# Kernel tuning notes

Measured on AMD Instinct MI355X. Metric: run time of the kernel, lower is better.

## Reference

```python
import jax, jax.numpy as jnp
import numpy as np

D_MODEL = 1024
N_HEADS = 16
D_HEAD = D_MODEL // N_HEADS


def setup_inputs() -> dict:
    key = jax.random.key(0)
    ks = jax.random.split(key, 11)
    B, S = 2, 2048
    s_in = 1.0 / np.sqrt(D_MODEL)
    return {
        "query": jax.random.normal(ks[0], (B, S, D_MODEL), jnp.float32),
        "key": jax.random.normal(ks[1], (B, S, D_MODEL), jnp.float32),
        "value": jax.random.normal(ks[2], (B, S, D_MODEL), jnp.float32),
        "Wq_w": jax.random.normal(ks[3], (D_MODEL, D_MODEL), jnp.float32) * s_in,
        "Wq_b": jax.random.normal(ks[4], (D_MODEL,), jnp.float32) * 0.01,
        "Wk_w": jax.random.normal(ks[5], (D_HEAD, D_MODEL), jnp.float32) * s_in,
        "Wk_b": jax.random.normal(ks[6], (D_HEAD,), jnp.float32) * 0.01,
        "Wv_w": jax.random.normal(ks[7], (D_HEAD, D_MODEL), jnp.float32) * s_in,
        "Wv_b": jax.random.normal(ks[8], (D_HEAD,), jnp.float32) * 0.01,
        "Wo_w": jax.random.normal(ks[9], (D_MODEL, D_MODEL), jnp.float32) * s_in,
        "Wo_b": jax.random.normal(ks[10], (D_MODEL,), jnp.float32) * 0.01,
    }


def reference(query, key, value, Wq_w, Wq_b, Wk_w, Wk_b, Wv_w, Wv_b, Wo_w, Wo_b):
    B, S, _ = query.shape
    # Q: per-head projection [B, H, S, dh]; K/V: single shared head [B, S, dh]
    Q = (query @ Wq_w.T + Wq_b).reshape(B, S, N_HEADS, D_HEAD).transpose(0, 2, 1, 3)
    K = key @ Wk_w.T + Wk_b      # [B, S, dh], shared across heads (MQA)
    V = value @ Wv_w.T + Wv_b    # [B, S, dh]
    scale = 1.0 / np.sqrt(D_HEAD).astype(np.float32)
    scores = jnp.einsum('bhqd,bkd->bhqk', Q, K) * scale  # [B, H, S, S]
    attn = jax.nn.softmax(scores, axis=-1)
    ctx = jnp.einsum('bhqk,bkd->bhqd', attn, V)           # [B, H, S, dh]
    ctx = ctx.transpose(0, 2, 1, 3).reshape(B, S, D_MODEL)
    out = ctx @ Wo_w.T + Wo_b
    return out, attn
```

## Files before the change

### kernel.cpp

```cpp
#include <hip/hip_runtime.h>
#include <hip/hip_bf16.h>
#include <math.h>

#define D_MODEL 1024
#define N_HEADS 16
#define D_HEAD 64
#define S_ 2048

typedef __attribute__((ext_vector_type(8))) short short8;
typedef __attribute__((ext_vector_type(4))) float f32x4;
typedef __attribute__((ext_vector_type(16))) float f32x16;

static __device__ inline short f2bf(float f) {
    union { __hip_bfloat16 h; short s; } u;
    u.h = __float2bfloat16(f);
    return u.s;
}

static __device__ inline f32x4 mfma16(short8 a, short8 b, f32x4 c) {
    return __builtin_amdgcn_mfma_f32_16x16x32_bf16(a, b, c, 0, 0, 0);
}
static __device__ inline f32x16 mfma32(short8 a, short8 b, f32x16 c) {
    return __builtin_amdgcn_mfma_f32_32x32x16_bf16(a, b, c, 0, 0, 0);
}
static __device__ inline f32x16 zero16() {
    f32x16 z;
#pragma unroll
    for (int i = 0; i < 16; i++) z[i] = 0.f;
    return z;
}

static __device__ inline void load_lds16(const void* g, void* l) {
    __builtin_amdgcn_global_load_lds(
        (const __attribute__((address_space(1))) unsigned int*)g,
        (__attribute__((address_space(3))) unsigned int*)l, 16, 0, 0);
}

__global__ __launch_bounds__(256)
void cvt_all(const float* __restrict__ q, const float* __restrict__ k,
             const float* __restrict__ v, const float* __restrict__ wq,
             const float* __restrict__ wk, const float* __restrict__ wv,
             const float* __restrict__ wo,
             short* dq, short* dk, short* dv, short* dwq, short* dwk,
             short* dwv, short* dwo) {
    size_t c = (size_t)blockIdx.x * 256 + threadIdx.x;
    const float* s; short* d; size_t off;
    if (c < 524288)        { s = q;  d = dq;  off = c; }
    else if (c < 1048576)  { s = k;  d = dk;  off = c - 524288; }
    else if (c < 1572864)  { s = v;  d = dv;  off = c - 1048576; }
    else if (c < 1703936)  { s = wq; d = dwq; off = c - 1572864; }
    else if (c < 1712128)  { s = wk; d = dwk; off = c - 1703936; }
    else if (c < 1720320)  { s = wv; d = dwv; off = c - 1712128; }
    else                   { s = wo; d = dwo; off = c - 1720320; }
    const f32x4* sp = (const f32x4*)(s + off * 8);
    f32x4 a = sp[0], b = sp[1];
    short8 o;
    o[0] = f2bf(a[0]); o[1] = f2bf(a[1]); o[2] = f2bf(a[2]); o[3] = f2bf(a[3]);
    o[4] = f2bf(b[0]); o[5] = f2bf(b[1]); o[6] = f2bf(b[2]); o[7] = f2bf(b[3]);
    *(short8*)(d + off * 8) = o;
}

template<int BM, int BN, int OUT_MODE>
__device__ __forceinline__ void gemm_body(
    const short* __restrict__ A, const short* __restrict__ Wb,
    const float* __restrict__ bias, void* __restrict__ Cv,
    int bx, int by, int M, int N, int K, float out_scale, char* lds)
{
    constexpr int NI = BM / 32, NJ = BN / 32;
    constexpr int AISS = BM / 32, WISS = BN / 32;
    char* As = lds;
    char* Ws = lds + 2 * BM * 128;
    const int t = threadIdx.x, lane = t & 63, w = t >> 6;
    const int wr = w >> 1, wc = w & 1, r15 = lane & 15, g = lane >> 4;
    const int m0 = by * BM, n0 = bx * BN;
    const size_t Kb2 = (size_t)K * 2;

    int aR[AISS], aC[AISS];
#pragma unroll
    for (int i = 0; i < AISS; i++) {
        int l = i * 4096 + t * 16;
        aR[i] = l >> 7;
        aC[i] = (l & 127) ^ (((l >> 7) & 7) << 4);
    }

    f32x4 acc[NI][NJ];
#pragma unroll
    for (int i = 0; i < NI; i++)
#pragma unroll
        for (int j = 0; j < NJ; j++) acc[i][j] = (f32x4){0.f, 0.f, 0.f, 0.f};

    const int nk = K / 64;
    auto stage = [&](int kt, int buf) {
        size_t kb = (size_t)kt * 128;
#pragma unroll
        for (int i = 0; i < AISS; i++)
            load_lds16((const char*)A + (size_t)(m0 + aR[i]) * Kb2 + kb + aC[i],
                       As + buf * (BM * 128) + i * 4096 + (w << 10));
#pragma unroll
        for (int i = 0; i < WISS; i++)
            load_lds16((const char*)Wb + (size_t)(n0 + aR[i]) * Kb2 + kb + aC[i],
                       Ws + buf * (BN * 128) + i * 4096 + (w << 10));
    };

    stage(0, 0);
    __syncthreads();
    int cur = 0;
    for (int kt = 0; kt < nk; kt++) {
        if (kt + 1 < nk) stage(kt + 1, cur ^ 1);
        const char* Ab = As + cur * (BM * 128);
        const char* Wbs = Ws + cur * (BN * 128);
#pragma unroll
        for (int kc = 0; kc < 2; kc++) {
            short8 af[NI], bw[NJ];
#pragma unroll
            for (int i = 0; i < NI; i++) {
                int r = wr * (16 * NI) + i * 16 + r15;
                af[i] = *(const short8*)(Ab + r * 128 + ((kc * 64 + g * 16) ^ ((r & 7) << 4)));
            }
#pragma unroll
            for (int j = 0; j < NJ; j++) {
                int r = wc * (16 * NJ) + j * 16 + r15;
                bw[j] = *(const short8*)(Wbs + r * 128 + ((kc * 64 + g * 16) ^ ((r & 7) << 4)));
            }
#pragma unroll
            for (int i = 0; i < NI; i++)
#pragma unroll
                for (int j = 0; j < NJ; j++)
                    acc[i][j] = mfma16(af[i], bw[j], acc[i][j]);
        }
        __syncthreads();
        cur ^= 1;
    }

#pragma unroll
    for (int i = 0; i < NI; i++) {
#pragma unroll
        for (int j = 0; j < NJ; j++) {
            int ncol = n0 + wc * (16 * NJ) + j * 16 + r15;
            float bv = bias[ncol];
#pragma unroll
            for (int reg = 0; reg < 4; reg++) {
                int mrow = m0 + wr * (16 * NI) + i * 16 + g * 4 + reg;
                float val = (acc[i][j][reg] + bv) * out_scale;
                if (OUT_MODE == 0) {
                    __builtin_nontemporal_store(val, (float*)Cv + (size_t)mrow * N + ncol);
                } else if (OUT_MODE == 1) {
                    ((short*)Cv)[(size_t)mrow * N + ncol] = f2bf(val);
                } else {
                    ((short*)Cv)[((((size_t)(mrow >> 11)) * 64 + ncol) << 11) +
                                 (mrow & 2047)] = f2bf(val);
                }
            }
        }
    }
}

__global__ __launch_bounds__(256)
void qkv_proj(const short* __restrict__ qin, const short* __restrict__ kin,
              const short* __restrict__ vin, const short* __restrict__ wqb,
              const short* __restrict__ wkb, const short* __restrict__ wvb,
              const float* __restrict__ bq, const float* __restrict__ bk,
              const float* __restrict__ bv,
              short* Qb, short* Kb, short* Vtb) {
    __shared__ char lds[65536];
    int bid = blockIdx.x;
    if (bid < 256)
        gemm_body<128, 128, 1>(qin, wqb, bq, Qb, bid & 7, bid >> 3,
                               4096, 1024, 1024, 0.18033688011112f, lds);
    else if (bid < 288)
        gemm_body<128, 64, 1>(kin, wkb, bk, Kb, 0, bid - 256,
                              4096, 64, 1024, 1.0f, lds);
    else
        gemm_body<128, 64, 2>(vin, wvb, bv, Vtb, 0, bid - 288,
                              4096, 64, 1024, 1.0f, lds);
}

__global__ __launch_bounds__(256)
void o_proj(const short* __restrict__ ctxb, const short* __restrict__ wob,
            const float* __restrict__ bo, float* __restrict__ out) {
    __shared__ char lds[65536];
    gemm_body<128, 128, 0>(ctxb, wob, bo, out, blockIdx.x & 7, blockIdx.x >> 3,
                           4096, 1024, 1024, 1.0f, lds);
}

__global__ __launch_bounds__(256)
void mqa_attn3(const short* __restrict__ Qb,
               const short* __restrict__ Kb,
               const short* __restrict__ Vtb,
               float* __restrict__ attn,
               short* __restrict__ ctxb)
{
    __shared__ short KB2[2][64 * 64];
    __shared__ short VB2[2][64 * 64];
    __shared__ short Ps[128 * 64];

    const int t = threadIdx.x, lane = t & 63, w = t >> 6;
    const int l31 = lane & 31, h5 = lane >> 5;
    const int bid = blockIdx.x;
    const int qt = bid & 15, h = (bid >> 4) & 15, b = bid >> 8;
    const int q0 = qt * 128;
    const int wq = w * 32;

    short8 aq[4];
    {
        const char* qbase = (const char*)(Qb +
            (size_t)(b * S_ + q0 + wq + l31) * D_MODEL + h * 64);
#pragma unroll
        for (int kc = 0; kc < 4; kc++)
            aq[kc] = *(const short8*)(qbase + kc * 32 + h5 * 16);
    }

    const int l0 = t * 16, l1 = l0 + 4096;
    const int row0 = l0 >> 7, row1 = l1 >> 7;
    const int ko0 = l0 ^ ((row0 & 7) << 4);
    const int ko1 = l1 ^ ((row1 & 7) << 4);
    const int vc0 = (l0 & 127) ^ ((row0 & 7) << 4);
    const int vc1 = (l1 & 127) ^ ((row1 & 7) << 4);
    const char* ktile0 = (const char*)(Kb + (size_t)b * S_ * 64);
    const char* vrow0 = (const char*)(Vtb + (((size_t)(b * 64 + row0)) << 11)) + vc0;
    const char* vrow1 = (const char*)(Vtb + (((size_t)(b * 64 + row1)) << 11)) + vc1;

#define STAGE_K(kti, buf) {                                                    \
        const char* kb_ = ktile0 + (size_t)(kti) * 8192;                       \
        load_lds16(kb_ + ko0, (char*)KB2 + (buf) * 8192 + (w << 10));          \
        load_lds16(kb_ + ko1, (char*)KB2 + (buf) * 8192 + 4096 + (w << 10)); }
#define STAGE_V(kti, buf) {                                                    \
        load_lds16(vrow0 + (size_t)(kti) * 128, (char*)VB2 + (buf) * 8192 + (w << 10)); \
        load_lds16(vrow1 + (size_t)(kti) * 128, (char*)VB2 + (buf) * 8192 + 4096 + (w << 10)); }
#define RD(base, r, cb) (*(const short8*)((const char*)(base) + (r) * 128 + ((cb) ^ (((r) & 7) << 4))))

    float lsum[16];
#pragma unroll
    for (int reg = 0; reg < 16; reg++) lsum[reg] = 0.f;

    int cur = 0;
    STAGE_K(0, 0);
    __syncthreads();
    for (int kti = 0; kti < 32; kti++) {
        if (kti + 1 < 32) STAGE_K(kti + 1, cur ^ 1);
        f32x16 s0 = zero16(), s1 = zero16();
#pragma unroll
        for (int kc = 0; kc < 4; kc++) {
            short8 k0 = RD(KB2[cur], l31, kc * 32 + h5 * 16);
            s0 = mfma32(aq[kc], k0, s0);
            short8 k1 = RD(KB2[cur], 32 + l31, kc * 32 + h5 * 16);
            s1 = mfma32(aq[kc], k1, s1);
        }
#pragma unroll
        for (int reg = 0; reg < 16; reg++)
            lsum[reg] += exp2f(s0[reg]) + exp2f(s1[reg]);
        __syncthreads();
        cur ^= 1;
    }

    float inv[16];
#pragma unroll
    for (int reg = 0; reg < 16; reg++) {
        float v = lsum[reg];
        v += __shfl_xor(v, 1); v += __shfl_xor(v, 2);
        v += __shfl_xor(v, 4); v += __shfl_xor(v, 8); v += __shfl_xor(v, 16);
        inv[reg] = 1.f / v;
    }

    f32x16 ctxA = zero16(), ctxB = zero16();
    float* attn_base = attn +
        (((size_t)((b * 16 + h) * 2048 + q0 + wq + 4 * h5)) << 11) + l31;

    cur = 0;
    STAGE_K(0, 0);
    STAGE_V(0, 0);
    __syncthreads();
    for (int kti = 0; kti < 32; kti++) {
        if (kti + 1 < 32) { STAGE_K(kti + 1, cur ^ 1); STAGE_V(kti + 1, cur ^ 1); }
        f32x16 s0 = zero16(), s1 = zero16();
#pragma unroll
        for (int kc = 0; kc < 4; kc++) {
            short8 k0 = RD(KB2[cur], l31, kc * 32 + h5 * 16);
            s0 = mfma32(aq[kc], k0, s0);
            short8 k1 = RD(KB2[cur], 32 + l31, kc * 32 + h5 * 16);
            s1 = mfma32(aq[kc], k1, s1);
        }
        float* arowptr = attn_base + (size_t)kti * 64;
#pragma unroll
        for (int reg = 0; reg < 16; reg++) {
            const int rloc = (reg & 3) + 8 * (reg >> 2);
            const int rps = wq + rloc + 4 * h5;
            float p0 = exp2f(s0[reg]) * inv[reg];
            __builtin_nontemporal_store(p0, arowptr + ((size_t)rloc << 11));
            *(short*)((char*)Ps + rps * 128 + ((l31 * 2) ^ ((rps & 7) << 4))) = f2bf(p0);
            float p1 = exp2f(s1[reg]) * inv[reg];
            __builtin_nontemporal_store(p1, arowptr + ((size_t)rloc << 11) + 32);
            *(short*)((char*)Ps + rps * 128 + ((64 + l31 * 2) ^ ((rps & 7) << 4))) = f2bf(p1);
        }
        short8 ap[4];
#pragma unroll
        for (int kc = 0; kc < 4; kc++)
            ap[kc] = RD(Ps, wq + l31, kc * 32 + h5 * 16);
#pragma unroll
        for (int kc = 0; kc < 4; kc++) {
            short8 v0 = RD(VB2[cur], l31, kc * 32 + h5 * 16);
            ctxA = mfma32(ap[kc], v0, ctxA);
            short8 v1 = RD(VB2[cur], 32 + l31, kc * 32 + h5 * 16);
            ctxB = mfma32(ap[kc], v1, ctxB);
        }
        __syncthreads();
        cur ^= 1;
    }

    const int tokbase = b * 2048 + q0 + wq + 4 * h5;
#pragma unroll
    for (int reg = 0; reg < 16; reg++) {
        const int rloc = (reg & 3) + 8 * (reg >> 2);
        size_t base = (size_t)(tokbase + rloc) * D_MODEL + h * 64 + l31;
        ctxb[base]      = f2bf(ctxA[reg]);
        ctxb[base + 32] = f2bf(ctxB[reg]);
    }
#undef STAGE_K
#undef STAGE_V
#undef RD
}

extern "C" void kernel_launch(void* const* d_in, const int* in_sizes, int n_in,
                              void* d_out, int out_size, void* d_ws, size_t ws_size,
                              hipStream_t stream) {
    const float* query = (const float*)d_in[0];
    const float* key   = (const float*)d_in[1];
    const float* value = (const float*)d_in[2];
    const float* Wq_w  = (const float*)d_in[3];
    const float* Wq_b  = (const float*)d_in[4];
    const float* Wk_w  = (const float*)d_in[5];
    const float* Wk_b  = (const float*)d_in[6];
    const float* Wv_w  = (const float*)d_in[7];
    const float* Wv_b  = (const float*)d_in[8];
    const float* Wo_w  = (const float*)d_in[9];
    const float* Wo_b  = (const float*)d_in[10];

    short* ws   = (short*)d_ws;
    short* qin  = ws;
    short* kin  = qin  + (size_t)4194304;
    short* vin  = kin  + (size_t)4194304;
    short* wqb  = vin  + (size_t)4194304;
    short* wkb  = wqb  + (size_t)1048576;
    short* wvb  = wkb  + (size_t)65536;
    short* wob  = wvb  + (size_t)65536;
    short* Qb   = wob  + (size_t)1048576;
    short* Kb   = Qb   + (size_t)4194304;
    short* Vtb  = Kb   + (size_t)262144;
    short* ctxb = Vtb  + (size_t)262144;

    float* out  = (float*)d_out;
    float* attn = out + (size_t)4096 * 1024;

    dim3 blk(256);

    cvt_all<<<dim3(7232), blk, 0, stream>>>(query, key, value, Wq_w, Wk_w, Wv_w,
                                            Wo_w, qin, kin, vin, wqb, wkb, wvb, wob);
    qkv_proj<<<dim3(320), blk, 0, stream>>>(qin, kin, vin, wqb, wkb, wvb,
                                            Wq_b, Wk_b, Wv_b, Qb, Kb, Vtb);
    mqa_attn3<<<dim3(512), blk, 0, stream>>>(Qb, Kb, Vtb, attn, ctxb);
    o_proj<<<dim3(256), blk, 0, stream>>>(ctxb, wob, Wo_b, out);
}
```

Baseline: 224.1 us.

## Read K/V MFMA fragments directly from global memory instead of LDS staging

The attention kernel no longer double-buffers K and V tiles into shared memory with async LDS loads and block-wide barriers. Each lane now loads its short8 MFMA operands straight from global memory, relying on L1/L2 caching because K/V are shared across all heads (MQA). This removes the per-tile __syncthreads and LDS traffic, but gives up explicit prefetching, so the MFMAs are now exposed to global-load latency.

```diff
diff --git a/kernel.cpp b/kernel.cpp
--- a/kernel.cpp
+++ b/kernel.cpp
@@ -184,14 +184,12 @@
 }
 
 __global__ __launch_bounds__(256)
-void mqa_attn3(const short* __restrict__ Qb,
+void mqa_attn4(const short* __restrict__ Qb,
                const short* __restrict__ Kb,
                const short* __restrict__ Vtb,
                float* __restrict__ attn,
                short* __restrict__ ctxb)
 {
-    __shared__ short KB2[2][64 * 64];
-    __shared__ short VB2[2][64 * 64];
     __shared__ short Ps[128 * 64];
 
     const int t = threadIdx.x, lane = t & 63, w = t >> 6;
@@ -210,47 +208,27 @@
             aq[kc] = *(const short8*)(qbase + kc * 32 + h5 * 16);
     }
 
-    const int l0 = t * 16, l1 = l0 + 4096;
-    const int row0 = l0 >> 7, row1 = l1 >> 7;
-    const int ko0 = l0 ^ ((row0 & 7) << 4);
-    const int ko1 = l1 ^ ((row1 & 7) << 4);
-    const int vc0 = (l0 & 127) ^ ((row0 & 7) << 4);
-    const int vc1 = (l1 & 127) ^ ((row1 & 7) << 4);
-    const char* ktile0 = (const char*)(Kb + (size_t)b * S_ * 64);
-    const char* vrow0 = (const char*)(Vtb + (((size_t)(b * 64 + row0)) << 11)) + vc0;
-    const char* vrow1 = (const char*)(Vtb + (((size_t)(b * 64 + row1)) << 11)) + vc1;
-
-#define STAGE_K(kti, buf) {                                                    \
-        const char* kb_ = ktile0 + (size_t)(kti) * 8192;                       \
-        load_lds16(kb_ + ko0, (char*)KB2 + (buf) * 8192 + (w << 10));          \
-        load_lds16(kb_ + ko1, (char*)KB2 + (buf) * 8192 + 4096 + (w << 10)); }
-#define STAGE_V(kti, buf) {                                                    \
-        load_lds16(vrow0 + (size_t)(kti) * 128, (char*)VB2 + (buf) * 8192 + (w << 10)); \
-        load_lds16(vrow1 + (size_t)(kti) * 128, (char*)VB2 + (buf) * 8192 + 4096 + (w << 10)); }
+    const short* kp = Kb + ((size_t)b * S_ + l31) * D_HEAD + h5 * 8;
+    const short* vp = Vtb + ((size_t)b * 64 + l31) * S_ + h5 * 8;
+
+#define KF(kti, half, kc) (*(const short8*)(kp + (kti) * 4096 + (half) * 2048 + (kc) * 16))
+#define VF(kti, half, kc) (*(const short8*)(vp + (half) * 65536 + (kti) * 64 + (kc) * 16))
 #define RD(base, r, cb) (*(const short8*)((const char*)(base) + (r) * 128 + ((cb) ^ (((r) & 7) << 4))))
 
     float lsum[16];
 #pragma unroll
     for (int reg = 0; reg < 16; reg++) lsum[reg] = 0.f;
 
-    int cur = 0;
-    STAGE_K(0, 0);
-    __syncthreads();
     for (int kti = 0; kti < 32; kti++) {
-        if (kti + 1 < 32) STAGE_K(kti + 1, cur ^ 1);
         f32x16 s0 = zero16(), s1 = zero16();
 #pragma unroll
         for (int kc = 0; kc < 4; kc++) {
-            short8 k0 = RD(KB2[cur], l31, kc * 32 + h5 * 16);
-            s0 = mfma32(aq[kc], k0, s0);
-            short8 k1 = RD(KB2[cur], 32 + l31, kc * 32 + h5 * 16);
-            s1 = mfma32(aq[kc], k1, s1);
+            s0 = mfma32(aq[kc], KF(kti, 0, kc), s0);
+            s1 = mfma32(aq[kc], KF(kti, 1, kc), s1);
         }
 #pragma unroll
         for (int reg = 0; reg < 16; reg++)
             lsum[reg] += exp2f(s0[reg]) + exp2f(s1[reg]);
-        __syncthreads();
-        cur ^= 1;
     }
 
     float inv[16];
@@ -266,19 +244,12 @@
     float* attn_base = attn +
         (((size_t)((b * 16 + h) * 2048 + q0 + wq + 4 * h5)) << 11) + l31;
 
-    cur = 0;
-    STAGE_K(0, 0);
-    STAGE_V(0, 0);
-    __syncthreads();
     for (int kti = 0; kti < 32; kti++) {
-        if (kti + 1 < 32) { STAGE_K(kti + 1, cur ^ 1); STAGE_V(kti + 1, cur ^ 1); }
         f32x16 s0 = zero16(), s1 = zero16();
 #pragma unroll
         for (int kc = 0; kc < 4; kc++) {
-            short8 k0 = RD(KB2[cur], l31, kc * 32 + h5 * 16);
-            s0 = mfma32(aq[kc], k0, s0);
-            short8 k1 = RD(KB2[cur], 32 + l31, kc * 32 + h5 * 16);
-            s1 = mfma32(aq[kc], k1, s1);
+            s0 = mfma32(aq[kc], KF(kti, 0, kc), s0);
+            s1 = mfma32(aq[kc], KF(kti, 1, kc), s1);
         }
         float* arowptr = attn_base + (size_t)kti * 64;
 #pragma unroll
@@ -298,13 +269,9 @@
             ap[kc] = RD(Ps, wq + l31, kc * 32 + h5 * 16);
 #pragma unroll
         for (int kc = 0; kc < 4; kc++) {
-            short8 v0 = RD(VB2[cur], l31, kc * 32 + h5 * 16);
-            ctxA = mfma32(ap[kc], v0, ctxA);
-            short8 v1 = RD(VB2[cur], 32 + l31, kc * 32 + h5 * 16);
-            ctxB = mfma32(ap[kc], v1, ctxB);
-        }
-        __syncthreads();
-        cur ^= 1;
+            ctxA = mfma32(ap[kc], VF(kti, 0, kc), ctxA);
+            ctxB = mfma32(ap[kc], VF(kti, 1, kc), ctxB);
+        }
     }
 
     const int tokbase = b * 2048 + q0 + wq + 4 * h5;
@@ -315,8 +282,8 @@
         ctxb[base]      = f2bf(ctxA[reg]);
         ctxb[base + 32] = f2bf(ctxB[reg]);
     }
-#undef STAGE_K
-#undef STAGE_V
+#undef KF
+#undef VF
 #undef RD
 }
 
@@ -357,6 +324,6 @@
                                             Wo_w, qin, kin, vin, wqb, wkb, wvb, wob);
     qkv_proj<<<dim3(320), blk, 0, stream>>>(qin, kin, vin, wqb, wkb, wvb,
                                             Wq_b, Wk_b, Wv_b, Qb, Kb, Vtb);
-    mqa_attn3<<<dim3(512), blk, 0, stream>>>(Qb, Kb, Vtb, attn, ctxb);
+    mqa_attn4<<<dim3(512), blk, 0, stream>>>(Qb, Kb, Vtb, attn, ctxb);
     o_proj<<<dim3(256), blk, 0, stream>>>(ctxb, wob, Wo_b, out);
 }
```

Result: slower. 262.4 us (+17.1%).
